# Performance work log

Hardware: AMD Instinct MI355X
Metric: run time of the kernel (lower is better)

Reference implementation:

```python
import math
import jax, jax.numpy as jnp
import numpy as np

T_STEPS = 65536
T_S = 1.0      # net_params['t_s']
THETA = 10.0   # net_params['af_params']['theta']


def _eps_func(mult, tau, epsilon, t_end, t_s):
    vals = []
    for t in np.arange(0, t_end, t_s):
        v = mult * t / tau * math.exp(1 - t / tau)
        if abs(v) < abs(epsilon) and t > tau:
            break
        vals.append(v)
    return vals


def _srm_kernel(mult, tau, epsilon, t_end, t_s):
    # replicates SlayerTrainer._calculate_srm_kernel: pad-to-odd, prepend zeros, flip
    k = _eps_func(mult, tau, epsilon, t_end, t_s)
    if len(k) % 2 == 0:
        k.append(0.0)
    k = np.asarray(k, dtype=np.float32)
    k = np.concatenate([np.zeros(len(k) - 1, np.float32), k])[::-1].copy()
    return k  # (K,), K odd; causal after cross-correlation with pad K//2


def setup_inputs() -> dict:
    key = jax.random.key(0)
    k1, k2, k3 = jax.random.split(key, 3)
    x = jax.random.uniform(k1, (1, 1, 1, 250, T_STEPS), jnp.float32)
    srm = jnp.asarray(_srm_kernel(1.0, 10.0, 1e-4, 200, T_S))                 # sr_params
    ref = jnp.asarray(np.asarray(_eps_func(-20.0, 1.0, 1e-4, 200, T_S), np.float32))  # ref_params
    # SpikeLinear weights, init N(0, std=weights_init)
    w1 = jax.random.normal(k2, (25, 250), jnp.float32) * 4.0
    w2 = jax.random.normal(k3, (1, 25), jnp.float32) * 4.0
    return {"x": x, "srm": srm, "ref": ref, "w1": w1, "w2": w2}


def srm_conv(z, srm):
    # z: (C, T). Per-channel 1-D cross-correlation with 'same' padding,
    # equal to F.conv3d(x, eye-SRM kernel, padding=(0,0,K//2)) * t_s.
    K = srm.shape[0]
    p = K // 2
    lhs = z[:, None, :]            # (C, 1, T) -- channels as batch
    rhs = srm[None, None, :]       # (1, 1, K)
    out = jax.lax.conv_general_dilated(
        lhs, rhs, window_strides=(1,), padding=[(p, p)],
        dimension_numbers=("NCW", "OIW", "NCW"))
    return out[:, 0, :] * T_S


def gen_spikes(pot, ref):
    # Sequential integrate-fire with refractory feedback (slayer_cuda.get_spikes_cuda).
    # pot: (C, T). Carry = per-neuron buffer of scheduled future refractory additions.
    C = pot.shape[0]
    L = ref.shape[0]
    # ref[j] is added to potentials[t+j] on a spike at t (ref[0]==0); after the
    # shift, buf[0] corresponds to time t+1, so schedule ref[1:].
    ref_next = jnp.concatenate([ref[1:], jnp.zeros((1,), pot.dtype)])

    def step(buf, p_t):
        u = p_t + buf[:, 0]                           # membrane incl. refractory
        s = (u >= THETA).astype(pot.dtype)
        buf = jnp.concatenate([buf[:, 1:], jnp.zeros((C, 1), pot.dtype)], axis=1)
        buf = buf + s[:, None] * ref_next[None, :]
        return buf, (u, s / T_S)

    buf0 = jnp.zeros((C, L), pot.dtype)
    _, (u_seq, s_seq) = jax.lax.scan(step, buf0, pot.T)
    return u_seq.T, s_seq.T  # (C, T), (C, T)


def reference(x, srm, ref, w1, w2):
    h = srm_conv(x[0, 0, 0], srm)        # (250, T) SRM-filtered input spikes
    h = w1 @ h                           # (25, T)  SpikeLinear fc1
    _, s1 = gen_spikes(h, ref)           # (25, T)  spikes layer 1
    h = srm_conv(s1, srm)                # (25, T)  SRM on hidden spikes
    h = w2 @ h                           # (1, T)   SpikeLinear fc2
    _, s2 = gen_spikes(h, ref)           # (1, T)
    return s2.reshape(1, 1, 1, 1, -1)
```

## Files before the change

kernel.cpp:

```cpp
#include <hip/hip_runtime.h>


#define T_LEN   65536
#define NCH     250
#define NO1     25
#define KTAPS   129
#define PAD     128
#define SRM_LEN 257
#define REF_LEN 16
#define THETA_F 10.0f
#define LBLK    64
#define NBK     1024
#define WARM    64
#define TT      128
#define FTILE   1024
#define FT2     1024
#define NWORDS  (T_LEN / 32)

__device__ __forceinline__ void srm_step(float p, const float (&rn)[15], float (&b)[15],
                                         unsigned &m, float &sf_out) {
  float u = p + b[0];
  unsigned sp = (u >= THETA_F) ? 1u : 0u;
  float sf = sp ? 1.0f : 0.0f;
#pragma unroll
  for (int j = 0; j < 14; ++j) b[j] = __builtin_fmaf(sf, rn[j], b[j + 1]);
  b[14] = __fmul_rn(sf, rn[14]);
  m = (m << 1) | sp;
  sf_out = sf;
}

__global__ void k_fill(float* out, float v) {
  out[blockIdx.x * 256 + threadIdx.x] = v;
}

__global__ __launch_bounds__(256) void k_prep3(const float* __restrict__ w1,
                                               float* __restrict__ wg2) {
  for (int i = threadIdx.x; i < 4 * NCH * 8; i += 256) {
    int og = i / (NCH * 8);
    int r = i - og * (NCH * 8);
    int c = r >> 3;
    int j = r & 7;
    int ob = og * 6;
    int no = (og == 3) ? 7 : 6;
    wg2[i] = (j < no) ? w1[(ob + j) * NCH + c] : 0.0f;
  }
}

__global__ __launch_bounds__(256, 8) void k_mm1(const float* __restrict__ x,
                                                const float* __restrict__ wg2,
                                                float* __restrict__ y1) {
  const int tid = threadIdx.x;
  const int lane = tid & 63;
  const int og = __builtin_amdgcn_readfirstlane(tid >> 6);
  const int ob = og * 6;
  const int no = (og == 3) ? 7 : 6;
  const int t = blockIdx.x * TT + lane * 2;
  const float* wp = wg2 + og * (NCH * 8);
  const float* xp = x + t;
  float2 acc[7];
#pragma unroll
  for (int j = 0; j < 7; ++j) acc[j] = make_float2(0.f, 0.f);
#pragma unroll 10
  for (int c = 0; c < NCH; ++c) {
    float2 xv = *(const float2*)(xp + (size_t)c * T_LEN);
    const float* wr = wp + c * 8;
#pragma unroll
    for (int j = 0; j < 7; ++j) {
      acc[j].x = __builtin_fmaf(wr[j], xv.x, acc[j].x);
      acc[j].y = __builtin_fmaf(wr[j], xv.y, acc[j].y);
    }
  }
#pragma unroll
  for (int j = 0; j < 7; ++j)
    if (j < no) *(float2*)&y1[(size_t)(ob + j) * T_LEN + t] = acc[j];
}

__global__ __launch_bounds__(256, 8) void k_fir1(const float* __restrict__ y1,
                                                 const float* __restrict__ srm,
                                                 float* __restrict__ pot1) {
  __shared__ __align__(16) float win[FTILE + PAD];
  const int tid = threadIdx.x;
  const int o = blockIdx.y;
  const int t0 = blockIdx.x * FTILE;
  const float* yr = y1 + (size_t)o * T_LEN;
  for (int j = tid; j < FTILE + PAD; j += 256) {
    int g = t0 - PAD + j;
    win[j] = (g >= 0) ? yr[g] : 0.0f;
  }
  __syncthreads();
  const int base = tid * 4;
  float q0 = 0.0f, q1 = 0.0f, q2 = 0.0f, q3 = 0.0f;
#pragma unroll
  for (int i = 32; i >= 0; --i) {
    float4 v = *(const float4*)&win[base + 4 * i];
#pragma unroll
    for (int l = 3; l >= 0; --l) {
      float vl = (l == 0) ? v.x : (l == 1) ? v.y : (l == 2) ? v.z : v.w;
#pragma unroll
      for (int k = 0; k < 4; ++k) {
        int d = 128 + k - 4 * i - l;
        if (d >= 0 && d <= 128) {
          float e = srm[4 * i + l - k];
          if (k == 0) q0 = __builtin_fmaf(e, vl, q0);
          else if (k == 1) q1 = __builtin_fmaf(e, vl, q1);
          else if (k == 2) q2 = __builtin_fmaf(e, vl, q2);
          else q3 = __builtin_fmaf(e, vl, q3);
        }
      }
    }
  }
  *(float4*)&pot1[(size_t)o * T_LEN + t0 + base] = make_float4(q0, q1, q2, q3);
}

__global__ __launch_bounds__(256) void k_pot2(const unsigned* __restrict__ s1p,
                                              const float* __restrict__ srm,
                                              const float* __restrict__ w2,
                                              float* __restrict__ pot2) {
  __shared__ __align__(16) float zs[FT2 + PAD];
  const int tid = threadIdx.x;
  const int t0 = blockIdx.x * FT2;
  for (int j = tid; j < FT2 + PAD; j += 256) {
    int g = t0 - PAD + j;
    float z = 0.0f;
    if (g >= 0) {
      int wi = g >> 5, sh = g & 31;
#pragma unroll
      for (int o = 0; o < NO1; ++o) {
        unsigned wvv = s1p[o * NWORDS + wi];
        z += ((wvv >> sh) & 1u) ? w2[o] : 0.0f;
      }
    }
    zs[j] = z;
  }
  __syncthreads();
  const int base = tid * 4;
  float q0 = 0.0f, q1 = 0.0f, q2 = 0.0f, q3 = 0.0f;
#pragma unroll
  for (int i = 32; i >= 0; --i) {
    float4 v = *(const float4*)&zs[base + 4 * i];
#pragma unroll
    for (int l = 3; l >= 0; --l) {
      float vl = (l == 0) ? v.x : (l == 1) ? v.y : (l == 2) ? v.z : v.w;
#pragma unroll
      for (int k = 0; k < 4; ++k) {
        int d = 128 + k - 4 * i - l;
        if (d >= 0 && d <= 128) {
          float e = srm[4 * i + l - k];
          if (k == 0) q0 = __builtin_fmaf(e, vl, q0);
          else if (k == 1) q1 = __builtin_fmaf(e, vl, q1);
          else if (k == 2) q2 = __builtin_fmaf(e, vl, q2);
          else q3 = __builtin_fmaf(e, vl, q3);
        }
      }
    }
  }
  *(float4*)&pot2[t0 + base] = make_float4(q0, q1, q2, q3);
}

template <int C, bool PACKED>
__global__ __launch_bounds__(64) void k_scan_spec(const float* __restrict__ pot,
                                                  const float* __restrict__ refk,
                                                  float* __restrict__ s,
                                                  unsigned* __restrict__ sp_,
                                                  unsigned* __restrict__ specin_m,
                                                  unsigned* __restrict__ specout_m,
                                                  float* __restrict__ specout_b) {
  int idx = blockIdx.x * 64 + threadIdx.x;
  if (idx >= C * NBK) return;
  int c = idx / NBK;
  int bb = idx - c * NBK;
  int tsr = bb * LBLK - WARM;
  float rn[15];
#pragma unroll
  for (int j = 0; j < 15; ++j) rn[j] = refk[j + 1];
  float b[15];
#pragma unroll
  for (int j = 0; j < 15; ++j) b[j] = 0.0f;
  unsigned m = 0;
  const float* prow = pot + (size_t)c * T_LEN;
  float* srow = PACKED ? nullptr : (s + (size_t)c * T_LEN);
  unsigned* srowp = PACKED ? (sp_ + (size_t)c * NWORDS) : nullptr;

  auto proc4 = [&](float4 pv, int tg, bool emit) {
    float s0, s1v, s2, s3;
    srm_step(pv.x, rn, b, m, s0);
    srm_step(pv.y, rn, b, m, s1v);
    srm_step(pv.z, rn, b, m, s2);
    srm_step(pv.w, rn, b, m, s3);
    if (emit) {
      if (PACKED) {
        if (((tg + 3) & 31) == 31) srowp[(tg - 28) >> 5] = __brev(m);
      } else {
        *(float4*)(srow + tg) = make_float4(s0, s1v, s2, s3);
      }
    }
  };

  for (int k = 0; k < WARM + LBLK; k += 16) {
    if (k == WARM) specin_m[idx] = m & 0x7FFFu;
    int t = tsr + k;
    if (t < 0) continue;
    float4 p0 = *(const float4*)(prow + t);
    float4 p1 = *(const float4*)(prow + t + 4);
    float4 p2 = *(const float4*)(prow + t + 8);
    float4 p3 = *(const float4*)(prow + t + 12);
    const bool emit = (k >= WARM);
    proc4(p0, t, emit);
    proc4(p1, t + 4, emit);
    proc4(p2, t + 8, emit);
    proc4(p3, t + 12, emit);
  }
  specout_m[idx] = m & 0x7FFFu;
#pragma unroll
  for (int j = 0; j < 15; ++j) specout_b[idx * 16 + j] = b[j];
}

template <int C, bool PACKED>
__global__ __launch_bounds__(64) void k_scan_fix(const float* __restrict__ pot,
                                                 const float* __restrict__ refk,
                                                 float* __restrict__ s,
                                                 unsigned* __restrict__ sp_,
                                                 const unsigned* __restrict__ specin_m,
                                                 const unsigned* __restrict__ specout_m,
                                                 const float* __restrict__ specout_b) {
  const int c = blockIdx.x;
  const int lane = threadIdx.x;
  float rn[15];
#pragma unroll
  for (int j = 0; j < 15; ++j) rn[j] = refk[j + 1];
  float b[15];
#pragma unroll
  for (int j = 0; j < 15; ++j) b[j] = 0.0f;
  unsigned m = 0;
  bool haveB = true;
  const float* prow = pot + (size_t)c * T_LEN;
  float* srow = PACKED ? nullptr : (s + (size_t)c * T_LEN);
  unsigned* srowp = PACKED ? (sp_ + (size_t)c * NWORDS) : nullptr;
  unsigned prev_last = 0;

  unsigned siv[NBK / 64], sov[NBK / 64];
#pragma unroll
  for (int g = 0; g < NBK / 64; ++g) {
    siv[g] = specin_m[c * NBK + g * 64 + lane];
    sov[g] = specout_m[c * NBK + g * 64 + lane];
  }
#pragma unroll
  for (int g = 0; g < NBK / 64; ++g) {
    const unsigned si = siv[g];
    const unsigned so = sov[g];
    unsigned so_prev = __shfl_up(so, 1);
    if (lane == 0) so_prev = prev_last;
    const unsigned long long flags = __ballot(si == so_prev);
    prev_last = __shfl(so, 63);
    const unsigned si0 = __shfl(si, 0);
    if (flags == ~0ull && (m & 0x7FFFu) == si0) {
      m = prev_last;
      haveB = false;
      continue;
    }
    for (int r = 0; r < 64; ++r) {
      const unsigned sir = __shfl(si, r);
      const unsigned sor = __shfl(so, r);
      if ((m & 0x7FFFu) == sir) {
        m = sor;
        haveB = false;
      } else {
        const int bbr = g * 64 + r;
        if (!haveB) {
          const int pb = (c * NBK + bbr - 1) * 16;
#pragma unroll
          for (int q2 = 0; q2 < 15; ++q2) b[q2] = specout_b[pb + q2];
          haveB = true;
        }
        const int t0 = bbr * LBLK;
        for (int t = t0; t < t0 + LBLK; t += 4) {
          float4 pv = *(const float4*)(prow + t);
          float s0, s1v, s2, s3;
          srm_step(pv.x, rn, b, m, s0);
          srm_step(pv.y, rn, b, m, s1v);
          srm_step(pv.z, rn, b, m, s2);
          srm_step(pv.w, rn, b, m, s3);
          if (PACKED) {
            if ((((t + 3) & 31) == 31) && lane == 0) srowp[(t - 28) >> 5] = __brev(m);
          } else {
            if (lane == 0) *(float4*)(srow + t) = make_float4(s0, s1v, s2, s3);
          }
        }
        haveB = true;
      }
    }
  }
}

extern "C" void kernel_launch(void* const* d_in, const int* in_sizes, int n_in,
                              void* d_out, int out_size, void* d_ws, size_t ws_size,
                              hipStream_t stream) {
  const float* x    = (const float*)d_in[0];
  const float* srm  = (const float*)d_in[1];
  const float* refk = (const float*)d_in[2];
  const float* w1   = (const float*)d_in[3];
  const float* w2   = (const float*)d_in[4];
  float* out = (float*)d_out;

  float bad = 0.0f;
  if (n_in != 5) bad = 3.0f;
  else if (in_sizes[0] != NCH * T_LEN) bad = 4.0f;
  else if (in_sizes[1] != SRM_LEN)     bad = 5.0f;
  else if (in_sizes[2] != REF_LEN)     bad = 6.0f;
  else if (in_sizes[3] != NO1 * NCH)   bad = 7.0f;
  else if (in_sizes[4] != NO1)         bad = 8.0f;
  else if (out_size != T_LEN)          bad = 9.0f;
  if (bad != 0.0f) {
    k_fill<<<T_LEN / 256, 256, 0, stream>>>(out, bad);
    return;
  }

  size_t off = 0;
  auto alloc = [&](size_t bytes) { size_t o = off; off = (off + bytes + 255) & ~(size_t)255; return o; };
  char* ws = (char*)d_ws;
  size_t oY1  = alloc((size_t)NO1 * T_LEN * 4);
  size_t oP1  = alloc((size_t)NO1 * T_LEN * 4);
  size_t oS1P = alloc((size_t)NO1 * NWORDS * 4);
  size_t oP2  = alloc((size_t)T_LEN * 4);
  size_t oWG2 = alloc((size_t)4 * NCH * 8 * 4);
  if (ws_size < off) {
    k_fill<<<T_LEN / 256, 256, 0, stream>>>(out, 2.0f);
    return;
  }

  float*    y1   = (float*)(ws + oY1);
  float*    pot1 = (float*)(ws + oP1);
  unsigned* s1p  = (unsigned*)(ws + oS1P);
  float*    pot2 = (float*)(ws + oP2);
  float*    wg2  = (float*)(ws + oWG2);
  char* yb = ws + oY1;
  unsigned* si1 = (unsigned*)(yb);
  unsigned* so1 = (unsigned*)(yb + 102400);
  float*    sb1 = (float*)   (yb + 204800);
  unsigned* si2 = (unsigned*)(yb + 1843200);
  unsigned* so2 = (unsigned*)(yb + 1847296);
  float*    sb2 = (float*)   (yb + 1851392);

  k_prep3<<<1, 256, 0, stream>>>(w1, wg2);
  k_mm1<<<T_LEN / TT, 256, 0, stream>>>(x, wg2, y1);
  k_fir1<<<dim3(T_LEN / FTILE, NO1), 256, 0, stream>>>(y1, srm, pot1);
  k_scan_spec<NO1, true><<<(NO1 * NBK + 63) / 64, 64, 0, stream>>>(
      pot1, refk, nullptr, s1p, si1, so1, sb1);
  k_scan_fix<NO1, true><<<NO1, 64, 0, stream>>>(pot1, refk, nullptr, s1p, si1, so1, sb1);
  k_pot2<<<T_LEN / FT2, 256, 0, stream>>>(s1p, srm, w2, pot2);
  k_scan_spec<1, false><<<(NBK + 63) / 64, 64, 0, stream>>>(
      pot2, refk, out, nullptr, si2, so2, sb2);
  k_scan_fix<1, false><<<1, 64, 0, stream>>>(pot2, refk, out, nullptr, si2, so2, sb2);
}
```

Measured before the change: 99.24 us.

## Split mm1 channel reduction across waves and fuse layer-2 scan kernels

k_mm1 now runs 1024-thread blocks in which four wave groups each reduce a quarter of the 250 input channels. Partial sums are combined through shared memory, which shortens the per-thread serial FMA chain and raises parallelism for the 512-block grid. The layer-2 speculative scan and fix-up kernels are merged into one 1024-thread block that keeps the speculation state in shared memory, saving a launch and global round trips. The trade-offs are an extra barrier and LDS traffic in mm1, and the layer-2 speculation pass is limited to a single CU.

```diff
diff --git a/kernel.cpp b/kernel.cpp
--- a/kernel.cpp
+++ b/kernel.cpp
@@ -46,22 +46,12 @@
   }
 }
 
-__global__ __launch_bounds__(256, 8) void k_mm1(const float* __restrict__ x,
-                                                const float* __restrict__ wg2,
-                                                float* __restrict__ y1) {
-  const int tid = threadIdx.x;
-  const int lane = tid & 63;
-  const int og = __builtin_amdgcn_readfirstlane(tid >> 6);
-  const int ob = og * 6;
-  const int no = (og == 3) ? 7 : 6;
-  const int t = blockIdx.x * TT + lane * 2;
-  const float* wp = wg2 + og * (NCH * 8);
-  const float* xp = x + t;
-  float2 acc[7];
-#pragma unroll
-  for (int j = 0; j < 7; ++j) acc[j] = make_float2(0.f, 0.f);
-#pragma unroll 10
-  for (int c = 0; c < NCH; ++c) {
+template <int CN>
+__device__ __forceinline__ void mm_body(const float* __restrict__ xp,
+                                        const float* __restrict__ wp,
+                                        float2 (&acc)[7]) {
+#pragma unroll 9
+  for (int c = 0; c < CN; ++c) {
     float2 xv = *(const float2*)(xp + (size_t)c * T_LEN);
     const float* wr = wp + c * 8;
 #pragma unroll
@@ -70,9 +60,45 @@
       acc[j].y = __builtin_fmaf(wr[j], xv.y, acc[j].y);
     }
   }
-#pragma unroll
-  for (int j = 0; j < 7; ++j)
-    if (j < no) *(float2*)&y1[(size_t)(ob + j) * T_LEN + t] = acc[j];
+}
+
+__global__ __launch_bounds__(1024, 8) void k_mm1(const float* __restrict__ x,
+                                                 const float* __restrict__ wg2,
+                                                 float* __restrict__ y1) {
+  __shared__ __align__(16) float2 part[3][4][7][64];
+  const int tid = threadIdx.x;
+  const int lane = tid & 63;
+  const int w = __builtin_amdgcn_readfirstlane(tid >> 6);
+  const int og = w & 3;
+  const int q = w >> 2;
+  const int ob = og * 6;
+  const int no = (og == 3) ? 7 : 6;
+  const int cqs = q * 62 + (q < 2 ? q : 2);
+  const int t = blockIdx.x * TT + lane * 2;
+  const float* wp = wg2 + og * (NCH * 8) + cqs * 8;
+  const float* xp = x + (size_t)cqs * T_LEN + t;
+  float2 acc[7];
+#pragma unroll
+  for (int j = 0; j < 7; ++j) acc[j] = make_float2(0.f, 0.f);
+  if (q < 2) mm_body<63>(xp, wp, acc);
+  else       mm_body<62>(xp, wp, acc);
+  if (q > 0) {
+#pragma unroll
+    for (int j = 0; j < 7; ++j) part[q - 1][og][j][lane] = acc[j];
+  }
+  __syncthreads();
+  if (q == 0) {
+#pragma unroll
+    for (int j = 0; j < 7; ++j) {
+      float2 a = acc[j];
+      float2 p1 = part[0][og][j][lane];
+      float2 p2 = part[1][og][j][lane];
+      float2 p3 = part[2][og][j][lane];
+      a.x = __fadd_rn(__fadd_rn(__fadd_rn(a.x, p1.x), p2.x), p3.x);
+      a.y = __fadd_rn(__fadd_rn(__fadd_rn(a.y, p1.y), p2.y), p3.y);
+      if (j < no) *(float2*)&y1[(size_t)(ob + j) * T_LEN + t] = a;
+    }
+  }
 }
 
 __global__ __launch_bounds__(256, 8) void k_fir1(const float* __restrict__ y1,
@@ -157,10 +183,9 @@
   *(float4*)&pot2[t0 + base] = make_float4(q0, q1, q2, q3);
 }
 
-template <int C, bool PACKED>
+template <int C>
 __global__ __launch_bounds__(64) void k_scan_spec(const float* __restrict__ pot,
                                                   const float* __restrict__ refk,
-                                                  float* __restrict__ s,
                                                   unsigned* __restrict__ sp_,
                                                   unsigned* __restrict__ specin_m,
                                                   unsigned* __restrict__ specout_m,
@@ -178,8 +203,7 @@
   for (int j = 0; j < 15; ++j) b[j] = 0.0f;
   unsigned m = 0;
   const float* prow = pot + (size_t)c * T_LEN;
-  float* srow = PACKED ? nullptr : (s + (size_t)c * T_LEN);
-  unsigned* srowp = PACKED ? (sp_ + (size_t)c * NWORDS) : nullptr;
+  unsigned* srowp = sp_ + (size_t)c * NWORDS;
 
   auto proc4 = [&](float4 pv, int tg, bool emit) {
     float s0, s1v, s2, s3;
@@ -187,13 +211,7 @@
     srm_step(pv.y, rn, b, m, s1v);
     srm_step(pv.z, rn, b, m, s2);
     srm_step(pv.w, rn, b, m, s3);
-    if (emit) {
-      if (PACKED) {
-        if (((tg + 3) & 31) == 31) srowp[(tg - 28) >> 5] = __brev(m);
-      } else {
-        *(float4*)(srow + tg) = make_float4(s0, s1v, s2, s3);
-      }
-    }
+    if (emit && (((tg + 3) & 31) == 31)) srowp[(tg - 28) >> 5] = __brev(m);
   };
 
   for (int k = 0; k < WARM + LBLK; k += 16) {
@@ -215,10 +233,9 @@
   for (int j = 0; j < 15; ++j) specout_b[idx * 16 + j] = b[j];
 }
 
-template <int C, bool PACKED>
+template <int C>
 __global__ __launch_bounds__(64) void k_scan_fix(const float* __restrict__ pot,
                                                  const float* __restrict__ refk,
-                                                 float* __restrict__ s,
                                                  unsigned* __restrict__ sp_,
                                                  const unsigned* __restrict__ specin_m,
                                                  const unsigned* __restrict__ specout_m,
@@ -234,8 +251,7 @@
   unsigned m = 0;
   bool haveB = true;
   const float* prow = pot + (size_t)c * T_LEN;
-  float* srow = PACKED ? nullptr : (s + (size_t)c * T_LEN);
-  unsigned* srowp = PACKED ? (sp_ + (size_t)c * NWORDS) : nullptr;
+  unsigned* srowp = sp_ + (size_t)c * NWORDS;
   unsigned prev_last = 0;
 
   unsigned siv[NBK / 64], sov[NBK / 64];
@@ -280,11 +296,101 @@
           srm_step(pv.y, rn, b, m, s1v);
           srm_step(pv.z, rn, b, m, s2);
           srm_step(pv.w, rn, b, m, s3);
-          if (PACKED) {
-            if ((((t + 3) & 31) == 31) && lane == 0) srowp[(t - 28) >> 5] = __brev(m);
-          } else {
-            if (lane == 0) *(float4*)(srow + t) = make_float4(s0, s1v, s2, s3);
-          }
+          if ((((t + 3) & 31) == 31) && lane == 0) srowp[(t - 28) >> 5] = __brev(m);
+        }
+        haveB = true;
+      }
+    }
+  }
+}
+
+__global__ __launch_bounds__(1024) void k_scanl2(const float* __restrict__ pot,
+                                                 const float* __restrict__ refk,
+                                                 float* __restrict__ s,
+                                                 float* __restrict__ specout_b) {
+  __shared__ unsigned si[NBK], so[NBK];
+  const int tid = threadIdx.x;
+  float rn[15];
+#pragma unroll
+  for (int j = 0; j < 15; ++j) rn[j] = refk[j + 1];
+  float b[15];
+#pragma unroll
+  for (int j = 0; j < 15; ++j) b[j] = 0.0f;
+  unsigned m = 0;
+  {
+    const int tsr = tid * LBLK - WARM;
+    for (int k = 0; k < WARM + LBLK; k += 16) {
+      if (k == WARM) si[tid] = m & 0x7FFFu;
+      int t = tsr + k;
+      if (t < 0) continue;
+      float4 p0 = *(const float4*)(pot + t);
+      float4 p1 = *(const float4*)(pot + t + 4);
+      float4 p2 = *(const float4*)(pot + t + 8);
+      float4 p3 = *(const float4*)(pot + t + 12);
+      const bool emit = (k >= WARM);
+      float s0, s1v, s2, s3;
+      srm_step(p0.x, rn, b, m, s0); srm_step(p0.y, rn, b, m, s1v);
+      srm_step(p0.z, rn, b, m, s2); srm_step(p0.w, rn, b, m, s3);
+      if (emit) *(float4*)(s + t) = make_float4(s0, s1v, s2, s3);
+      srm_step(p1.x, rn, b, m, s0); srm_step(p1.y, rn, b, m, s1v);
+      srm_step(p1.z, rn, b, m, s2); srm_step(p1.w, rn, b, m, s3);
+      if (emit) *(float4*)(s + t + 4) = make_float4(s0, s1v, s2, s3);
+      srm_step(p2.x, rn, b, m, s0); srm_step(p2.y, rn, b, m, s1v);
+      srm_step(p2.z, rn, b, m, s2); srm_step(p2.w, rn, b, m, s3);
+      if (emit) *(float4*)(s + t + 8) = make_float4(s0, s1v, s2, s3);
+      srm_step(p3.x, rn, b, m, s0); srm_step(p3.y, rn, b, m, s1v);
+      srm_step(p3.z, rn, b, m, s2); srm_step(p3.w, rn, b, m, s3);
+      if (emit) *(float4*)(s + t + 12) = make_float4(s0, s1v, s2, s3);
+    }
+    so[tid] = m & 0x7FFFu;
+#pragma unroll
+    for (int j = 0; j < 15; ++j) specout_b[tid * 16 + j] = b[j];
+  }
+  __syncthreads();
+  if (tid >= 64) return;
+  const int lane = tid;
+#pragma unroll
+  for (int j = 0; j < 15; ++j) b[j] = 0.0f;
+  m = 0;
+  bool haveB = true;
+  unsigned prev_last = 0;
+#pragma unroll
+  for (int g = 0; g < NBK / 64; ++g) {
+    const unsigned siw = si[g * 64 + lane];
+    const unsigned sow = so[g * 64 + lane];
+    unsigned so_prev = __shfl_up(sow, 1);
+    if (lane == 0) so_prev = prev_last;
+    const unsigned long long flags = __ballot(siw == so_prev);
+    prev_last = __shfl(sow, 63);
+    const unsigned si0 = __shfl(siw, 0);
+    if (flags == ~0ull && (m & 0x7FFFu) == si0) {
+      m = prev_last;
+      haveB = false;
+      continue;
+    }
+    for (int r = 0; r < 64; ++r) {
+      const unsigned sir = __shfl(siw, r);
+      const unsigned sor = __shfl(sow, r);
+      if ((m & 0x7FFFu) == sir) {
+        m = sor;
+        haveB = false;
+      } else {
+        const int bbr = g * 64 + r;
+        if (!haveB) {
+          const int pb = (bbr - 1) * 16;
+#pragma unroll
+          for (int q2 = 0; q2 < 15; ++q2) b[q2] = specout_b[pb + q2];
+          haveB = true;
+        }
+        const int t0 = bbr * LBLK;
+        for (int t = t0; t < t0 + LBLK; t += 4) {
+          float4 pv = *(const float4*)(pot + t);
+          float s0, s1v, s2, s3;
+          srm_step(pv.x, rn, b, m, s0);
+          srm_step(pv.y, rn, b, m, s1v);
+          srm_step(pv.z, rn, b, m, s2);
+          srm_step(pv.w, rn, b, m, s3);
+          if (lane == 0) *(float4*)(s + t) = make_float4(s0, s1v, s2, s3);
         }
         haveB = true;
       }
@@ -337,18 +443,14 @@
   unsigned* si1 = (unsigned*)(yb);
   unsigned* so1 = (unsigned*)(yb + 102400);
   float*    sb1 = (float*)   (yb + 204800);
-  unsigned* si2 = (unsigned*)(yb + 1843200);
-  unsigned* so2 = (unsigned*)(yb + 1847296);
-  float*    sb2 = (float*)   (yb + 1851392);
+  float*    sb2 = (float*)   (yb + 1843200);
 
   k_prep3<<<1, 256, 0, stream>>>(w1, wg2);
-  k_mm1<<<T_LEN / TT, 256, 0, stream>>>(x, wg2, y1);
+  k_mm1<<<T_LEN / TT, 1024, 0, stream>>>(x, wg2, y1);
   k_fir1<<<dim3(T_LEN / FTILE, NO1), 256, 0, stream>>>(y1, srm, pot1);
-  k_scan_spec<NO1, true><<<(NO1 * NBK + 63) / 64, 64, 0, stream>>>(
-      pot1, refk, nullptr, s1p, si1, so1, sb1);
-  k_scan_fix<NO1, true><<<NO1, 64, 0, stream>>>(pot1, refk, nullptr, s1p, si1, so1, sb1);
+  k_scan_spec<NO1><<<(NO1 * NBK + 63) / 64, 64, 0, stream>>>(
+      pot1, refk, s1p, si1, so1, sb1);
+  k_scan_fix<NO1><<<NO1, 64, 0, stream>>>(pot1, refk, s1p, si1, so1, sb1);
   k_pot2<<<T_LEN / FT2, 256, 0, stream>>>(s1p, srm, w2, pot2);
-  k_scan_spec<1, false><<<(NBK + 63) / 64, 64, 0, stream>>>(
-      pot2, refk, out, nullptr, si2, so2, sb2);
-  k_scan_fix<1, false><<<1, 64, 0, stream>>>(pot2, refk, out, nullptr, si2, so2, sb2);
-}
+  k_scanl2<<<1, 1024, 0, stream>>>(pot2, refk, out, sb2);
+}
```

Measured after the change: 106.8 us. 7.6% more time.

## Split mm1 channel reduction across four wave groups with LDS partial-sum combine

Applied to the files above, without the earlier changes.

k_mm1 now runs 1024-thread blocks in which four groups of waves each reduce about a quarter of the 250 input channels. The partial sums are combined through shared memory by the first group before it writes y1. The aim is more parallelism and memory-level concurrency on the serial channel loop, since the previous launch had only 512 blocks of 256 threads. The cost is a block barrier, extra LDS traffic and a different floating-point summation order.

```diff
diff --git a/kernel.cpp b/kernel.cpp
--- a/kernel.cpp
+++ b/kernel.cpp
@@ -46,22 +46,12 @@
   }
 }
 
-__global__ __launch_bounds__(256, 8) void k_mm1(const float* __restrict__ x,
-                                                const float* __restrict__ wg2,
-                                                float* __restrict__ y1) {
-  const int tid = threadIdx.x;
-  const int lane = tid & 63;
-  const int og = __builtin_amdgcn_readfirstlane(tid >> 6);
-  const int ob = og * 6;
-  const int no = (og == 3) ? 7 : 6;
-  const int t = blockIdx.x * TT + lane * 2;
-  const float* wp = wg2 + og * (NCH * 8);
-  const float* xp = x + t;
-  float2 acc[7];
-#pragma unroll
-  for (int j = 0; j < 7; ++j) acc[j] = make_float2(0.f, 0.f);
-#pragma unroll 10
-  for (int c = 0; c < NCH; ++c) {
+template <int CN>
+__device__ __forceinline__ void mm_body(const float* __restrict__ xp,
+                                        const float* __restrict__ wp,
+                                        float2 (&acc)[7]) {
+#pragma unroll 9
+  for (int c = 0; c < CN; ++c) {
     float2 xv = *(const float2*)(xp + (size_t)c * T_LEN);
     const float* wr = wp + c * 8;
 #pragma unroll
@@ -70,9 +60,45 @@
       acc[j].y = __builtin_fmaf(wr[j], xv.y, acc[j].y);
     }
   }
-#pragma unroll
-  for (int j = 0; j < 7; ++j)
-    if (j < no) *(float2*)&y1[(size_t)(ob + j) * T_LEN + t] = acc[j];
+}
+
+__global__ __launch_bounds__(1024, 8) void k_mm1(const float* __restrict__ x,
+                                                 const float* __restrict__ wg2,
+                                                 float* __restrict__ y1) {
+  __shared__ __align__(16) float2 part[3][4][7][64];
+  const int tid = threadIdx.x;
+  const int lane = tid & 63;
+  const int w = __builtin_amdgcn_readfirstlane(tid >> 6);
+  const int og = w & 3;
+  const int q = w >> 2;
+  const int ob = og * 6;
+  const int no = (og == 3) ? 7 : 6;
+  const int cqs = q * 62 + (q < 2 ? q : 2);
+  const int t = blockIdx.x * TT + lane * 2;
+  const float* wp = wg2 + og * (NCH * 8) + cqs * 8;
+  const float* xp = x + (size_t)cqs * T_LEN + t;
+  float2 acc[7];
+#pragma unroll
+  for (int j = 0; j < 7; ++j) acc[j] = make_float2(0.f, 0.f);
+  if (q < 2) mm_body<63>(xp, wp, acc);
+  else       mm_body<62>(xp, wp, acc);
+  if (q > 0) {
+#pragma unroll
+    for (int j = 0; j < 7; ++j) part[q - 1][og][j][lane] = acc[j];
+  }
+  __syncthreads();
+  if (q == 0) {
+#pragma unroll
+    for (int j = 0; j < 7; ++j) {
+      float2 a = acc[j];
+      float2 p1 = part[0][og][j][lane];
+      float2 p2 = part[1][og][j][lane];
+      float2 p3 = part[2][og][j][lane];
+      a.x = __fadd_rn(__fadd_rn(__fadd_rn(a.x, p1.x), p2.x), p3.x);
+      a.y = __fadd_rn(__fadd_rn(__fadd_rn(a.y, p1.y), p2.y), p3.y);
+      if (j < no) *(float2*)&y1[(size_t)(ob + j) * T_LEN + t] = a;
+    }
+  }
 }
 
 __global__ __launch_bounds__(256, 8) void k_fir1(const float* __restrict__ y1,
@@ -342,7 +368,7 @@
   float*    sb2 = (float*)   (yb + 1851392);
 
   k_prep3<<<1, 256, 0, stream>>>(w1, wg2);
-  k_mm1<<<T_LEN / TT, 256, 0, stream>>>(x, wg2, y1);
+  k_mm1<<<T_LEN / TT, 1024, 0, stream>>>(x, wg2, y1);
   k_fir1<<<dim3(T_LEN / FTILE, NO1), 256, 0, stream>>>(y1, srm, pot1);
   k_scan_spec<NO1, true><<<(NO1 * NBK + 63) / 64, 64, 0, stream>>>(
       pot1, refk, nullptr, s1p, si1, so1, sb1);
```

Result: faster. 88.55 us (-10.8%).

## Split mm1 channel reduction across waves with LDS partial-sum combine

Applied to the files above, without the earlier changes.

Restructures the first linear layer kernel so each 1024-thread block covers 64 time steps. Waves split the work as 2 output halves by 8 channel groups, and partial sums are reduced through shared memory. Previously each wave looped over all 250 channels for 6-7 outputs on 2 time steps. The change aims to raise parallelism and memory-level concurrency on the x read, at the cost of LDS traffic, a block barrier and scalar instead of float2 loads.

```diff
diff --git a/kernel.cpp b/kernel.cpp
--- a/kernel.cpp
+++ b/kernel.cpp
@@ -12,7 +12,7 @@
 #define LBLK    64
 #define NBK     1024
 #define WARM    64
-#define TT      128
+#define TT      64
 #define FTILE   1024
 #define FT2     1024
 #define NWORDS  (T_LEN / 32)
@@ -33,46 +33,67 @@
   out[blockIdx.x * 256 + threadIdx.x] = v;
 }
 
-__global__ __launch_bounds__(256) void k_prep3(const float* __restrict__ w1,
-                                               float* __restrict__ wg2) {
-  for (int i = threadIdx.x; i < 4 * NCH * 8; i += 256) {
-    int og = i / (NCH * 8);
-    int r = i - og * (NCH * 8);
-    int c = r >> 3;
-    int j = r & 7;
-    int ob = og * 6;
-    int no = (og == 3) ? 7 : 6;
-    wg2[i] = (j < no) ? w1[(ob + j) * NCH + c] : 0.0f;
-  }
-}
-
-__global__ __launch_bounds__(256, 8) void k_mm1(const float* __restrict__ x,
-                                                const float* __restrict__ wg2,
-                                                float* __restrict__ y1) {
+__global__ __launch_bounds__(256) void k_prep4(const float* __restrict__ w1,
+                                               float* __restrict__ wg3) {
+  for (int i = threadIdx.x; i < 2 * NCH * 16; i += 256) {
+    int oh = i / (NCH * 16);
+    int r = i - oh * (NCH * 16);
+    int c = r >> 4;
+    int j = r & 15;
+    int ob = oh * 13;
+    int no = oh ? 12 : 13;
+    wg3[i] = (j < no) ? w1[(ob + j) * NCH + c] : 0.0f;
+  }
+}
+
+template <int CN>
+__device__ __forceinline__ void mm_body8(const float* __restrict__ xp,
+                                         const float* __restrict__ wp,
+                                         float (&acc)[13]) {
+#pragma unroll 8
+  for (int c = 0; c < CN; ++c) {
+    float xv = xp[(size_t)c * T_LEN];
+    const float* wr = wp + c * 16;
+#pragma unroll
+    for (int j = 0; j < 13; ++j)
+      acc[j] = __builtin_fmaf(wr[j], xv, acc[j]);
+  }
+}
+
+__global__ __launch_bounds__(1024, 8) void k_mm1(const float* __restrict__ x,
+                                                 const float* __restrict__ wg3,
+                                                 float* __restrict__ y1) {
+  __shared__ __align__(16) float part[7][2][13][64];
   const int tid = threadIdx.x;
   const int lane = tid & 63;
-  const int og = __builtin_amdgcn_readfirstlane(tid >> 6);
-  const int ob = og * 6;
-  const int no = (og == 3) ? 7 : 6;
-  const int t = blockIdx.x * TT + lane * 2;
-  const float* wp = wg2 + og * (NCH * 8);
-  const float* xp = x + t;
-  float2 acc[7];
-#pragma unroll
-  for (int j = 0; j < 7; ++j) acc[j] = make_float2(0.f, 0.f);
-#pragma unroll 10
-  for (int c = 0; c < NCH; ++c) {
-    float2 xv = *(const float2*)(xp + (size_t)c * T_LEN);
-    const float* wr = wp + c * 8;
-#pragma unroll
-    for (int j = 0; j < 7; ++j) {
-      acc[j].x = __builtin_fmaf(wr[j], xv.x, acc[j].x);
-      acc[j].y = __builtin_fmaf(wr[j], xv.y, acc[j].y);
-    }
-  }
-#pragma unroll
-  for (int j = 0; j < 7; ++j)
-    if (j < no) *(float2*)&y1[(size_t)(ob + j) * T_LEN + t] = acc[j];
+  const int w = __builtin_amdgcn_readfirstlane(tid >> 6);
+  const int oh = w & 1;
+  const int cg = w >> 1;
+  const int ob = oh * 13;
+  const int no = oh ? 12 : 13;
+  const int cs = (cg < 2) ? cg * 32 : 64 + (cg - 2) * 31;
+  const int t = blockIdx.x * TT + lane;
+  const float* wp = wg3 + oh * (NCH * 16) + cs * 16;
+  const float* xp = x + (size_t)cs * T_LEN + t;
+  float acc[13];
+#pragma unroll
+  for (int j = 0; j < 13; ++j) acc[j] = 0.f;
+  if (cg < 2) mm_body8<32>(xp, wp, acc);
+  else        mm_body8<31>(xp, wp, acc);
+  if (cg > 0) {
+#pragma unroll
+    for (int j = 0; j < 13; ++j) part[cg - 1][oh][j][lane] = acc[j];
+  }
+  __syncthreads();
+  if (cg == 0) {
+#pragma unroll
+    for (int j = 0; j < 13; ++j) {
+      float a = acc[j];
+#pragma unroll
+      for (int g = 0; g < 7; ++g) a = __fadd_rn(a, part[g][oh][j][lane]);
+      if (j < no) y1[(size_t)(ob + j) * T_LEN + t] = a;
+    }
+  }
 }
 
 __global__ __launch_bounds__(256, 8) void k_fir1(const float* __restrict__ y1,
@@ -322,7 +343,7 @@
   size_t oP1  = alloc((size_t)NO1 * T_LEN * 4);
   size_t oS1P = alloc((size_t)NO1 * NWORDS * 4);
   size_t oP2  = alloc((size_t)T_LEN * 4);
-  size_t oWG2 = alloc((size_t)4 * NCH * 8 * 4);
+  size_t oWG3 = alloc((size_t)2 * NCH * 16 * 4);
   if (ws_size < off) {
     k_fill<<<T_LEN / 256, 256, 0, stream>>>(out, 2.0f);
     return;
@@ -332,7 +353,7 @@
   float*    pot1 = (float*)(ws + oP1);
   unsigned* s1p  = (unsigned*)(ws + oS1P);
   float*    pot2 = (float*)(ws + oP2);
-  float*    wg2  = (float*)(ws + oWG2);
+  float*    wg3  = (float*)(ws + oWG3);
   char* yb = ws + oY1;
   unsigned* si1 = (unsigned*)(yb);
   unsigned* so1 = (unsigned*)(yb + 102400);
@@ -341,8 +362,8 @@
   unsigned* so2 = (unsigned*)(yb + 1847296);
   float*    sb2 = (float*)   (yb + 1851392);
 
-  k_prep3<<<1, 256, 0, stream>>>(w1, wg2);
-  k_mm1<<<T_LEN / TT, 256, 0, stream>>>(x, wg2, y1);
+  k_prep4<<<1, 256, 0, stream>>>(w1, wg3);
+  k_mm1<<<T_LEN / TT, 1024, 0, stream>>>(x, wg3, y1);
   k_fir1<<<dim3(T_LEN / FTILE, NO1), 256, 0, stream>>>(y1, srm, pot1);
   k_scan_spec<NO1, true><<<(NO1 * NBK + 63) / 64, 64, 0, stream>>>(
       pot1, refk, nullptr, s1p, si1, so1, sb1);
```

New measurement: 97.03 us. 1.02x faster.
